# Kernel tuning notes

Hardware: AMD Instinct MI355X
Metric: run time of the kernel (lower is better)

## Reference

```python
import jax, jax.numpy as jnp
import numpy as np

B, C, F, H, W, K = 8, 1, 64, 256, 256, 3
PAD = [(1, 1), (1, 1)]
DN = ('NCHW', 'OIHW', 'NCHW')


def _conv(x, w):
    # Conv2d(1->F, k=3, pad=1, no bias): x [B,1,H,W], w [F,1,3,3] -> [B,F,H,W]
    return jax.lax.conv_general_dilated(x, w, (1, 1), PAD, dimension_numbers=DN)


def _conv_t(u, w):
    # ConvTranspose2d(F->1, k=3, pad=1, stride=1) with shared weight == conv with
    # spatially-flipped kernel, in/out swapped, padding k-1-p = 1.
    wt = jnp.flip(w, axis=(-2, -1)).transpose(1, 0, 2, 3)  # [1,F,3,3]
    return jax.lax.conv_general_dilated(u, wt, (1, 1), PAD, dimension_numbers=DN)


def _op_norm2(w):
    # Power iteration for ||conv_t(conv(.))|| on an image of shape (1,H,W), max 300 iters, tol 1e-4.
    tol = jnp.float32(1e-4)
    x0 = jnp.ones((1, C, H, W), jnp.float32)
    x0 = x0 / jnp.linalg.norm(x0.reshape(-1))

    def cond(s):
        k, x, val, rel = s
        return jnp.logical_and(k < 300, rel >= tol)

    def body(s):
        k, x, val, rel = s
        x2 = _conv_t(_conv(x, w), w)
        v2 = jnp.linalg.norm(x2.reshape(-1))
        r2 = jnp.abs(v2 - val) / val
        return (k + 1, x2 / v2, v2, r2)

    _, _, val, _ = jax.lax.while_loop(
        cond, body, (0, x0, jnp.float32(1.0), jnp.array(jnp.inf, jnp.float32)))
    return jax.lax.stop_gradient(val)  # torch runs this under no_grad


def setup_inputs() -> dict:
    key = jax.random.key(0)
    ks = jax.random.split(key, 6)
    x_in = jax.random.uniform(ks[0], (B, C, H, W), jnp.float32)
    u_in = jax.random.normal(ks[1], (B, F, H, W), jnp.float32)
    bias = jax.random.normal(ks[2], (B, H * W), jnp.float32)
    beta = jnp.ones((1,), jnp.float32)
    lambd = jnp.ones((1,), jnp.float32)
    HtH_diag = jax.random.uniform(ks[3], (H * W,), jnp.float32)
    w = jax.random.normal(ks[4], (F, C, K, K), jnp.float32) * 0.1
    log_sigma = jnp.zeros((1,), jnp.float32)
    return {"x_in": x_in, "u_in": u_in, "bias": bias, "beta": beta,
            "lambd": lambd, "HtH_diag": HtH_diag, "w": w, "log_sigma": log_sigma}


def reference(x_in, u_in, bias, beta, lambd, HtH_diag, w, log_sigma):
    lip2 = _op_norm2(w)
    sigma = jnp.exp(log_sigma) + 0.05                 # [1]
    tau = 0.99 / (beta / 2 + sigma * lip2)            # [1]
    # H_star_H acts on flattened image: diagonal linear operator
    h = (x_in.reshape(x_in.shape[0], -1) * HtH_diag).reshape(x_in.shape)
    Dx = x_in - tau * h - tau * _conv_t(u_in, w) + tau * bias.reshape(x_in.shape)
    output0 = jnp.clip(Dx, 0.0, 1.0)
    Du = 2.0 * sigma * _conv(output0, w) - sigma * _conv(x_in, w) + u_in
    output1 = jnp.clip(Du, -lambd, lambd)
    return (output0, output1)
```

## Files before the change

kernel.cpp:

```cpp
#include <hip/hip_runtime.h>
#include <math.h>

#define IMH 256
#define IMW 256
#define NBT 8
#define NF  64
#define HW  65536

#define TSZ 16
#define MB 10
#define NBATCH 30
#define HALO (2*MB)
#define BROW 68
#define BUFSZ (60*BROW + 8)

#define NG0 8
#define FG0 (NF / NG0)

#define WS_SM   0
#define WS_K5   81
#define WS_ET   106
#define WS_EB   111
#define WS_EL   116
#define WS_ER   121
#define WS_C4   126
#define WS_LIP2 431
#define WS_TAU  432
#define WS_SIGMA 433
#define WS_ST_K    434
#define WS_ST_VAL  435
#define WS_ST_STOP 436

__global__ void setup_kernel(const float* __restrict__ w, float* __restrict__ ws) {
    int t = threadIdx.x;
    __shared__ float smS[81];
    if (t < 81) {
        int a = t / 9, bq = t % 9;
        int dry = a / 3 - 1, drx = a % 3 - 1;
        int dqy = bq / 3 - 1, dqx = bq % 3 - 1;
        int r_idx = (1 - dry) * 3 + (1 - drx);
        int q_idx = (dqy + 1) * 3 + (dqx + 1);
        float s = 0.f;
        for (int f = 0; f < NF; ++f) s += w[f * 9 + r_idx] * w[f * 9 + q_idx];
        smS[t] = s;
        ws[WS_SM + t] = s;
    }
    __syncthreads();
    if (t < 25) {
        int dy = t / 5 - 2, dx = t % 5 - 2;
        float k = 0.f;
        for (int a = 0; a < 9; ++a) {
            int dry = a / 3 - 1, drx = a % 3 - 1;
            for (int bq = 0; bq < 9; ++bq) {
                int dqy = bq / 3 - 1, dqx = bq % 3 - 1;
                if (dry + dqy == dy && drx + dqx == dx) k += smS[a * 9 + bq];
            }
        }
        ws[WS_K5 + t] = k;
    }
    if (t == 0) {
        for (int dd = 0; dd < 5; ++dd) {
            int dx = dd - 2;
            float et = 0.f, eb = 0.f, el = 0.f, er = 0.f;
            for (int dr = -1; dr <= 1; ++dr) {
                int dq = dx - dr;
                if (dq < -1 || dq > 1) continue;
                et += smS[(0 * 3 + dr + 1) * 9 + (2 * 3 + dq + 1)];
                eb += smS[(2 * 3 + dr + 1) * 9 + (0 * 3 + dq + 1)];
                el += smS[((dr + 1) * 3 + 0) * 9 + ((dq + 1) * 3 + 2)];
                er += smS[((dr + 1) * 3 + 2) * 9 + ((dq + 1) * 3 + 0)];
            }
            ws[WS_ET + dd] = et;
            ws[WS_EB + dd] = eb;
            ws[WS_EL + dd] = el;
            ws[WS_ER + dd] = er;
        }
        ws[WS_C4 + 0] = smS[0 * 9 + 8];
        ws[WS_C4 + 1] = smS[2 * 9 + 6];
        ws[WS_C4 + 2] = smS[6 * 9 + 2];
        ws[WS_C4 + 3] = smS[8 * 9 + 0];
        ws[WS_ST_K] = 0.f;
        ws[WS_ST_VAL] = 1.0f;
        ws[WS_ST_STOP] = 0.f;
    }
}

__global__ __launch_bounds__(256) void pi_batch_kernel(
    float* __restrict__ ws, float* __restrict__ gbuf,
    float* __restrict__ part, int batch) {
    __shared__ float bufA[BUFSZ];
    __shared__ float bufB[BUFSZ];
    __shared__ float sred[4];
    const int tid = threadIdx.x;
    const int bid = blockIdx.x;
    const int wid = tid >> 6;
    const int lane = tid & 63;
    const int q = tid & 15;
    const int strip = tid >> 4;
    const int tx = bid & 15;
    const int ty = bid >> 4;
    const float* gin = gbuf + ((batch & 1) ? HW : 0);
    float* gout      = gbuf + ((batch & 1) ? 0 : HW);

    if (batch > 0 && ws[WS_ST_STOP] != 0.f) return;

    if (bid == 0 && batch > 0) {
        float k_it = ws[WS_ST_K];
        float val  = ws[WS_ST_VAL];
        float nprev = 1.0f;
        float newstop = 0.f;
        const float* pb = part + (size_t)((batch - 1) * MB) * 1024;
        for (int s = 0; s < MB; ++s) {
            const float* pp = pb + (size_t)s * 1024;
            float sm = pp[tid] + pp[tid + 256] + pp[tid + 512] + pp[tid + 768];
#pragma unroll
            for (int o = 32; o > 0; o >>= 1) sm += __shfl_down(sm, o, 64);
            if (lane == 0) sred[wid] = sm;
            __syncthreads();
            float tot = sred[0] + sred[1] + sred[2] + sred[3];
            __syncthreads();
            float n = sqrtf(tot);
            float v = n / nprev;
            nprev = n;
            float rel = fabsf(v - val) / val;
            val = v;
            k_it += 1.f;
            if (rel < 1e-4f || k_it >= 300.f) { newstop = 1.f; break; }
        }
        if (tid == 0) {
            ws[WS_ST_K] = k_it;
            ws[WS_ST_VAL] = val;
            ws[WS_ST_STOP] = newstop;
        }
        __syncthreads();
    }

    float k5[25];
#pragma unroll
    for (int i = 0; i < 25; ++i) k5[i] = ws[WS_K5 + i];
    float et[5], eb[5], el[5], er[5], c4[4];
#pragma unroll
    for (int i = 0; i < 5; ++i) {
        et[i] = ws[WS_ET + i]; eb[i] = ws[WS_EB + i];
        el[i] = ws[WS_EL + i]; er[i] = ws[WS_ER + i];
    }
#pragma unroll
    for (int i = 0; i < 4; ++i) c4[i] = ws[WS_C4 + i];

    float inv_n;
    if (batch == 0) {
        inv_n = 1.0f / 256.0f;
    } else {
        const float* pp = part + (size_t)(batch * MB - 1) * 1024;
        float s = pp[tid] + pp[tid + 256] + pp[tid + 512] + pp[tid + 768];
#pragma unroll
        for (int o = 32; o > 0; o >>= 1) s += __shfl_down(s, o, 64);
        if (lane == 0) sred[wid] = s;
        __syncthreads();
        inv_n = 1.0f / sqrtf(sred[0] + sred[1] + sred[2] + sred[3]);
        __syncthreads();
    }

    for (int i = tid; i < BUFSZ; i += 256) {
        float v = 0.f;
        if (i >= 4) {
            int cell = i - 4;
            int r = cell / BROW, c = cell - r * BROW;
            if (r < 60 && c < 64) {
                int gy = ty * 16 - 22 + r;
                int gx = tx * 16 - 24 + c;
                if ((unsigned)gy < IMH && (unsigned)gx < IMW)
                    v = (batch == 0) ? inv_n : gin[gy * IMW + gx] * inv_n;
            }
        }
        bufA[i] = v;
        bufB[i] = 0.f;
    }
    __syncthreads();

    const bool active = (strip < 14);
    const int r0 = 2 + 4 * strip;
    const int gy0 = ty * 16 - 22 + r0;
    const int gx0 = tx * 16 - 24 + 4 * q;
    bool iny[4], bt[4], bb[4];
#pragma unroll
    for (int k = 0; k < 4; ++k) {
        int gy = gy0 + k;
        iny[k] = ((unsigned)gy < IMH);
        bt[k] = (gy == 0);
        bb[k] = (gy == IMH - 1);
    }
    bool inx[4];
#pragma unroll
    for (int i = 0; i < 4; ++i) inx[i] = ((unsigned)(gx0 + i) < IMW);
    const bool bL = (gx0 == 0);
    const bool bR = (gx0 + 3 == IMW - 1);
    const bool central = (q >= 6 && q < 10) && (strip >= 5 && strip < 9);
    const int wrow_lo = 2 + 16 * wid;
    const int wrow_hi = (wrow_lo + 16 < 58) ? wrow_lo + 16 : 58;

    float* cur = bufA;
    float* nxt = bufB;
#pragma unroll 1
    for (int s = 0; s < MB; ++s) {
        float pv = 0.f;
        const int lo = 2 + 2 * (s + 1);
        const int hi = 58 - 2 * (s + 1);
        const bool wave_need = (wrow_lo < hi) && (wrow_hi > lo);
        if (active && wave_need) {
            float win[8][8];
            const int base = 4 + (r0 - 2) * BROW + 4 * q;
#pragma unroll
            for (int m = 0; m < 8; ++m) {
                float4 a = *(const float4*)&cur[base + m * BROW];
                float2 lo2 = *(const float2*)&cur[base + m * BROW - 2];
                float2 hi2 = *(const float2*)&cur[base + m * BROW + 4];
                win[m][0] = lo2.x; win[m][1] = lo2.y;
                win[m][2] = a.x;  win[m][3] = a.y;
                win[m][4] = a.z;  win[m][5] = a.w;
                win[m][6] = hi2.x; win[m][7] = hi2.y;
            }
            float z[4][4];
#pragma unroll
            for (int k = 0; k < 4; ++k) {
#pragma unroll
                for (int i = 0; i < 4; ++i) z[k][i] = 0.f;
#pragma unroll
                for (int j = 0; j < 5; ++j) {
#pragma unroll
                    for (int dx = 0; dx < 5; ++dx) {
                        const float kv = k5[j * 5 + dx];
                        z[k][0] += kv * win[k + j][0 + dx];
                        z[k][1] += kv * win[k + j][1 + dx];
                        z[k][2] += kv * win[k + j][2 + dx];
                        z[k][3] += kv * win[k + j][3 + dx];
                    }
                }
            }
#pragma unroll
            for (int k = 0; k < 4; ++k) {
                if (bt[k]) {
#pragma unroll
                    for (int i = 0; i < 4; ++i) {
                        float c = 0.f;
#pragma unroll
                        for (int d = 0; d < 5; ++d) c += et[d] * win[k + 2][i + d];
                        z[k][i] -= c;
                    }
                }
                if (bb[k]) {
#pragma unroll
                    for (int i = 0; i < 4; ++i) {
                        float c = 0.f;
#pragma unroll
                        for (int d = 0; d < 5; ++d) c += eb[d] * win[k + 2][i + d];
                        z[k][i] -= c;
                    }
                }
            }
            if (bL) {
#pragma unroll
                for (int k = 0; k < 4; ++k) {
                    float c = 0.f;
#pragma unroll
                    for (int j = 0; j < 5; ++j) c += el[j] * win[k + j][2];
                    z[k][0] -= c;
                    if (bt[k]) z[k][0] += c4[0] * win[k + 2][2];
                    if (bb[k]) z[k][0] += c4[2] * win[k + 2][2];
                }
            }
            if (bR) {
#pragma unroll
                for (int k = 0; k < 4; ++k) {
                    float c = 0.f;
#pragma unroll
                    for (int j = 0; j < 5; ++j) c += er[j] * win[k + j][5];
                    z[k][3] -= c;
                    if (bt[k]) z[k][3] += c4[1] * win[k + 2][5];
                    if (bb[k]) z[k][3] += c4[3] * win[k + 2][5];
                }
            }
#pragma unroll
            for (int k = 0; k < 4; ++k) {
                float4 o;
                o.x = (iny[k] && inx[0]) ? z[k][0] : 0.f;
                o.y = (iny[k] && inx[1]) ? z[k][1] : 0.f;
                o.z = (iny[k] && inx[2]) ? z[k][2] : 0.f;
                o.w = (iny[k] && inx[3]) ? z[k][3] : 0.f;
                *(float4*)&nxt[4 + (r0 + k) * BROW + 4 * q] = o;
                if (central)
                    pv += o.x * o.x + o.y * o.y + o.z * o.z + o.w * o.w;
            }
        }
#pragma unroll
        for (int o = 32; o > 0; o >>= 1) pv += __shfl_down(pv, o, 64);
        if (lane == 0)
            part[(size_t)(batch * MB + s) * 1024 + (bid << 2) + wid] = pv;
        __syncthreads();
        float* tmp = cur; cur = nxt; nxt = tmp;
    }

    if (tid < 64) {
        int rr = tid >> 2, cq = tid & 3;
        float4 v = *(const float4*)&cur[4 + (22 + rr) * BROW + 24 + 4 * cq];
        int gy = ty * 16 + rr, gx = tx * 16 + 4 * cq;
        *(float4*)&gout[gy * IMW + gx] = v;
    }
}

__global__ __launch_bounds__(256) void finalize_kernel(
    float* __restrict__ ws, const float* __restrict__ part,
    const float* __restrict__ beta, const float* __restrict__ log_sigma) {
    __shared__ float sr[4];
    const int tid = threadIdx.x;
    const int lane = tid & 63;
    const int wid = tid >> 6;
    float k_it = ws[WS_ST_K];
    float val  = ws[WS_ST_VAL];
    const float stop = ws[WS_ST_STOP];
    if (stop == 0.f) {
        float nprev = 1.0f;
        const float* pb = part + (size_t)((NBATCH - 1) * MB) * 1024;
        for (int s = 0; s < MB; ++s) {
            const float* pp = pb + (size_t)s * 1024;
            float sm = pp[tid] + pp[tid + 256] + pp[tid + 512] + pp[tid + 768];
#pragma unroll
            for (int o = 32; o > 0; o >>= 1) sm += __shfl_down(sm, o, 64);
            if (lane == 0) sr[wid] = sm;
            __syncthreads();
            float tot = sr[0] + sr[1] + sr[2] + sr[3];
            __syncthreads();
            float n = sqrtf(tot);
            float v = n / nprev;
            nprev = n;
            float rel = fabsf(v - val) / val;
            val = v;
            k_it += 1.f;
            if (rel < 1e-4f || k_it >= 300.f) break;
        }
    }
    if (tid == 0) {
        float lip2 = val;
        float sigma = expf(log_sigma[0]) + 0.05f;
        float tau = 0.99f / (beta[0] * 0.5f + sigma * lip2);
        ws[WS_LIP2] = lip2;
        ws[WS_TAU] = tau;
        ws[WS_SIGMA] = sigma;
    }
}

__global__ __launch_bounds__(256) void out0_part_kernel(
    const float* __restrict__ u_in, const float* __restrict__ w,
    float* __restrict__ part0) {
    const int tid = threadIdx.x;
    const int lane = tid & 63;
    const int wid = tid >> 6;
    const int y = blockIdx.x * 4 + wid;
    const int g = blockIdx.y;
    const int b = blockIdx.z;
    const int x0 = lane * 4;
    float4 ct = {0.f, 0.f, 0.f, 0.f};
    const float* ub = u_in + ((size_t)b * NF + g * FG0) * HW;
    const float* wg = w + g * FG0 * 9;
#pragma unroll 4
    for (int f = 0; f < FG0; ++f) {
        const float* uf = ub + (size_t)f * HW;
        const float* wf = wg + f * 9;
#pragma unroll
        for (int dy = -1; dy <= 1; ++dy) {
            int yy = y + dy;
            float4 v = {0.f, 0.f, 0.f, 0.f};
            if ((unsigned)yy < IMH)
                v = *(const float4*)(uf + yy * IMW + x0);
            float m1 = __shfl_up(v.w, 1);
            if (lane == 0) m1 = 0.f;
            float p4 = __shfl_down(v.x, 1);
            if (lane == 63) p4 = 0.f;
            const float w2 = wf[(1 - dy) * 3 + 2];
            const float w1 = wf[(1 - dy) * 3 + 1];
            const float w0 = wf[(1 - dy) * 3 + 0];
            ct.x += w2 * m1  + w1 * v.x + w0 * v.y;
            ct.y += w2 * v.x + w1 * v.y + w0 * v.z;
            ct.z += w2 * v.y + w1 * v.z + w0 * v.w;
            ct.w += w2 * v.z + w1 * v.w + w0 * p4;
        }
    }
    *(float4*)(part0 + ((size_t)(g * NBT + b)) * HW + y * IMW + x0) = ct;
}

__global__ __launch_bounds__(256) void out0_combine_kernel(
    const float* __restrict__ x_in, const float* __restrict__ bias,
    const float* __restrict__ HtH, const float* __restrict__ ws,
    const float* __restrict__ part0, float* __restrict__ out0) {
    const int tid = threadIdx.x;
    const int lane = tid & 63;
    const int wid = tid >> 6;
    const int y = blockIdx.x * 4 + wid;
    const int b = blockIdx.y;
    const int x0 = lane * 4;
    const int p = y * IMW + x0;
    const float tau = ws[WS_TAU];
    float4 ct = {0.f, 0.f, 0.f, 0.f};
#pragma unroll
    for (int g = 0; g < NG0; ++g) {
        const float4 pv = *(const float4*)(part0 + ((size_t)(g * NBT + b)) * HW + p);
        ct.x += pv.x; ct.y += pv.y; ct.z += pv.z; ct.w += pv.w;
    }
    const float4 xi = *(const float4*)(x_in + (size_t)b * HW + p);
    const float4 hh = *(const float4*)(HtH + p);
    const float4 bs = *(const float4*)(bias + (size_t)b * HW + p);
    float4 o;
    o.x = fminf(fmaxf(xi.x - tau * (hh.x * xi.x) - tau * ct.x + tau * bs.x, 0.f), 1.f);
    o.y = fminf(fmaxf(xi.y - tau * (hh.y * xi.y) - tau * ct.y + tau * bs.y, 0.f), 1.f);
    o.z = fminf(fmaxf(xi.z - tau * (hh.z * xi.z) - tau * ct.z + tau * bs.z, 0.f), 1.f);
    o.w = fminf(fmaxf(xi.w - tau * (hh.w * xi.w) - tau * ct.w + tau * bs.w, 0.f), 1.f);
    *(float4*)(out0 + (size_t)b * HW + p) = o;
}

__global__ __launch_bounds__(256) void out1_kernel(
    const float* __restrict__ x_in, const float* __restrict__ u_in,
    const float* __restrict__ lambd, const float* __restrict__ w,
    const float* __restrict__ ws, const float* __restrict__ out0,
    float* __restrict__ out1) {
    const int tid = threadIdx.x;
    const int lane = tid & 63;
    const int wid = tid >> 6;
    const int y = blockIdx.x * 4 + wid;
    const int f = blockIdx.y;
    const int b = blockIdx.z;
    const int x0 = lane * 4;
    const float sigma = ws[WS_SIGMA];
    const float lam = lambd[0];
    const float* wf = w + f * 9;
    float wr[9];
#pragma unroll
    for (int i = 0; i < 9; ++i) wr[i] = wf[i];
    const float* o0 = out0 + (size_t)b * HW;
    const float* xb = x_in + (size_t)b * HW;
    float4 s1 = {0.f, 0.f, 0.f, 0.f};
    float4 s2 = {0.f, 0.f, 0.f, 0.f};
#pragma unroll
    for (int dy = -1; dy <= 1; ++dy) {
        int yy = y + dy;
        float4 a = {0.f, 0.f, 0.f, 0.f};
        float4 c = {0.f, 0.f, 0.f, 0.f};
        if ((unsigned)yy < IMH) {
            a = *(const float4*)(o0 + yy * IMW + x0);
            c = *(const float4*)(xb + yy * IMW + x0);
        }
        float am1 = __shfl_up(a.w, 1);  if (lane == 0) am1 = 0.f;
        float ap4 = __shfl_down(a.x, 1); if (lane == 63) ap4 = 0.f;
        float cm1 = __shfl_up(c.w, 1);  if (lane == 0) cm1 = 0.f;
        float cp4 = __shfl_down(c.x, 1); if (lane == 63) cp4 = 0.f;
        const float w0 = wr[(dy + 1) * 3 + 0];
        const float w1 = wr[(dy + 1) * 3 + 1];
        const float w2 = wr[(dy + 1) * 3 + 2];
        s1.x += w0 * am1 + w1 * a.x + w2 * a.y;
        s1.y += w0 * a.x + w1 * a.y + w2 * a.z;
        s1.z += w0 * a.y + w1 * a.z + w2 * a.w;
        s1.w += w0 * a.z + w1 * a.w + w2 * ap4;
        s2.x += w0 * cm1 + w1 * c.x + w2 * c.y;
        s2.y += w0 * c.x + w1 * c.y + w2 * c.z;
        s2.z += w0 * c.y + w1 * c.z + w2 * c.w;
        s2.w += w0 * c.z + w1 * c.w + w2 * cp4;
    }
    const size_t idx = (size_t)(b * NF + f) * HW + y * IMW + x0;
    const float4 uq = *(const float4*)(u_in + idx);
    float4 o;
    o.x = fminf(fmaxf(2.f * sigma * s1.x - sigma * s2.x + uq.x, -lam), lam);
    o.y = fminf(fmaxf(2.f * sigma * s1.y - sigma * s2.y + uq.y, -lam), lam);
    o.z = fminf(fmaxf(2.f * sigma * s1.z - sigma * s2.z + uq.z, -lam), lam);
    o.w = fminf(fmaxf(2.f * sigma * s1.w - sigma * s2.w + uq.w, -lam), lam);
    *(float4*)(out1 + idx) = o;
}

extern "C" void kernel_launch(void* const* d_in, const int* in_sizes, int n_in,
                              void* d_out, int out_size, void* d_ws, size_t ws_size,
                              hipStream_t stream) {
    const float* x_in = (const float*)d_in[0];
    const float* u_in = (const float*)d_in[1];
    const float* bias = (const float*)d_in[2];
    const float* beta = (const float*)d_in[3];
    const float* lambd = (const float*)d_in[4];
    const float* HtH = (const float*)d_in[5];
    const float* w = (const float*)d_in[6];
    const float* log_sigma = (const float*)d_in[7];
    float* ws = (float*)d_ws;
    float* out0 = (float*)d_out;
    float* out1 = out0 + (size_t)NBT * HW;
    float* gbuf = out1;
    float* part = out1 + 2 * HW;
    float* part0 = part + (size_t)300 * 1024;

    setup_kernel<<<1, 128, 0, stream>>>(w, ws);
    for (int b = 0; b < NBATCH; ++b)
        pi_batch_kernel<<<256, 256, 0, stream>>>(ws, gbuf, part, b);
    finalize_kernel<<<1, 256, 0, stream>>>(ws, part, beta, log_sigma);
    out0_part_kernel<<<dim3(IMH / 4, NG0, NBT), 256, 0, stream>>>(u_in, w, part0);
    out0_combine_kernel<<<dim3(IMH / 4, NBT), 256, 0, stream>>>(x_in, bias, HtH, ws, part0, out0);
    out1_kernel<<<dim3(IMH / 4, NF, NBT), 256, 0, stream>>>(x_in, u_in, lambd, w, ws, out0, out1);
}
```

Baseline: 397.8 us.

## Fold out0 partial conv into power-iteration launches and double PI threads

The separate out0_part_kernel is removed. Its 2048 row-group blocks are now spread across the 30 power-iteration launches as 69 extra blocks each, so that streaming u_in can overlap with the latency-bound stencil iterations. The power-iteration blocks also go from 256 to 512 threads, with each thread computing 2 output rows instead of 4, and the partial-norm layout and reductions widen to match. The risk is that the extra blocks compete with the stencil blocks for CUs and memory bandwidth, and the bigger blocks add reduction and sync overhead.

```diff
diff --git a/kernel.cpp b/kernel.cpp
--- a/kernel.cpp
+++ b/kernel.cpp
@@ -14,8 +14,13 @@
 #define BROW 68
 #define BUFSZ (60*BROW + 8)
 
+#define PIT 512
+#define NPART 2048
+
 #define NG0 8
 #define FG0 (NF / NG0)
+#define OB_TOTAL 2048
+#define OBPB 69
 
 #define WS_SM   0
 #define WS_K5   81
@@ -85,14 +90,58 @@
     }
 }
 
-__global__ __launch_bounds__(256) void pi_batch_kernel(
+__global__ __launch_bounds__(PIT) void pi_batch_kernel(
     float* __restrict__ ws, float* __restrict__ gbuf,
-    float* __restrict__ part, int batch) {
+    float* __restrict__ part, float* __restrict__ part0,
+    const float* __restrict__ u_in, const float* __restrict__ w,
+    int batch) {
     __shared__ float bufA[BUFSZ];
     __shared__ float bufB[BUFSZ];
-    __shared__ float sred[4];
+    __shared__ float sred[8];
     const int tid = threadIdx.x;
     const int bid = blockIdx.x;
+
+    if (bid >= 256) {
+        const int obi = batch * OBPB + (bid - 256);
+        if (obi < OB_TOTAL) {
+            const int yb = obi & 31;
+            const int g = (obi >> 5) & 7;
+            const int b = obi >> 8;
+            const int lane = tid & 63;
+            const int wd = tid >> 6;
+            const int y = yb * 8 + wd;
+            const int x0 = lane * 4;
+            float4 ct = {0.f, 0.f, 0.f, 0.f};
+            const float* ub = u_in + ((size_t)b * NF + g * FG0) * HW;
+            const float* wg = w + g * FG0 * 9;
+#pragma unroll 4
+            for (int f = 0; f < FG0; ++f) {
+                const float* uf = ub + (size_t)f * HW;
+                const float* wf = wg + f * 9;
+#pragma unroll
+                for (int dy = -1; dy <= 1; ++dy) {
+                    int yy = y + dy;
+                    float4 v = {0.f, 0.f, 0.f, 0.f};
+                    if ((unsigned)yy < IMH)
+                        v = *(const float4*)(uf + yy * IMW + x0);
+                    float m1 = __shfl_up(v.w, 1);
+                    if (lane == 0) m1 = 0.f;
+                    float p4 = __shfl_down(v.x, 1);
+                    if (lane == 63) p4 = 0.f;
+                    const float w2 = wf[(1 - dy) * 3 + 2];
+                    const float w1 = wf[(1 - dy) * 3 + 1];
+                    const float w0 = wf[(1 - dy) * 3 + 0];
+                    ct.x += w2 * m1  + w1 * v.x + w0 * v.y;
+                    ct.y += w2 * v.x + w1 * v.y + w0 * v.z;
+                    ct.z += w2 * v.y + w1 * v.z + w0 * v.w;
+                    ct.w += w2 * v.z + w1 * v.w + w0 * p4;
+                }
+            }
+            *(float4*)(part0 + ((size_t)(g * NBT + b)) * HW + y * IMW + x0) = ct;
+        }
+        return;
+    }
+
     const int wid = tid >> 6;
     const int lane = tid & 63;
     const int q = tid & 15;
@@ -109,15 +158,16 @@
         float val  = ws[WS_ST_VAL];
         float nprev = 1.0f;
         float newstop = 0.f;
-        const float* pb = part + (size_t)((batch - 1) * MB) * 1024;
+        const float* pb = part + (size_t)((batch - 1) * MB) * NPART;
         for (int s = 0; s < MB; ++s) {
-            const float* pp = pb + (size_t)s * 1024;
-            float sm = pp[tid] + pp[tid + 256] + pp[tid + 512] + pp[tid + 768];
+            const float* pp = pb + (size_t)s * NPART;
+            float sm = pp[tid] + pp[tid + 512] + pp[tid + 1024] + pp[tid + 1536];
 #pragma unroll
             for (int o = 32; o > 0; o >>= 1) sm += __shfl_down(sm, o, 64);
             if (lane == 0) sred[wid] = sm;
             __syncthreads();
-            float tot = sred[0] + sred[1] + sred[2] + sred[3];
+            float tot = sred[0] + sred[1] + sred[2] + sred[3]
+                      + sred[4] + sred[5] + sred[6] + sred[7];
             __syncthreads();
             float n = sqrtf(tot);
             float v = n / nprev;
@@ -151,17 +201,18 @@
     if (batch == 0) {
         inv_n = 1.0f / 256.0f;
     } else {
-        const float* pp = part + (size_t)(batch * MB - 1) * 1024;
-        float s = pp[tid] + pp[tid + 256] + pp[tid + 512] + pp[tid + 768];
+        const float* pp = part + (size_t)(batch * MB - 1) * NPART;
+        float s = pp[tid] + pp[tid + 512] + pp[tid + 1024] + pp[tid + 1536];
 #pragma unroll
         for (int o = 32; o > 0; o >>= 1) s += __shfl_down(s, o, 64);
         if (lane == 0) sred[wid] = s;
         __syncthreads();
-        inv_n = 1.0f / sqrtf(sred[0] + sred[1] + sred[2] + sred[3]);
+        inv_n = 1.0f / sqrtf(sred[0] + sred[1] + sred[2] + sred[3]
+                           + sred[4] + sred[5] + sred[6] + sred[7]);
         __syncthreads();
     }
 
-    for (int i = tid; i < BUFSZ; i += 256) {
+    for (int i = tid; i < BUFSZ; i += PIT) {
         float v = 0.f;
         if (i >= 4) {
             int cell = i - 4;
@@ -178,13 +229,13 @@
     }
     __syncthreads();
 
-    const bool active = (strip < 14);
-    const int r0 = 2 + 4 * strip;
+    const bool active = (strip < 28);
+    const int r0 = 2 + 2 * strip;
     const int gy0 = ty * 16 - 22 + r0;
     const int gx0 = tx * 16 - 24 + 4 * q;
-    bool iny[4], bt[4], bb[4];
-#pragma unroll
-    for (int k = 0; k < 4; ++k) {
+    bool iny[2], bt[2], bb[2];
+#pragma unroll
+    for (int k = 0; k < 2; ++k) {
         int gy = gy0 + k;
         iny[k] = ((unsigned)gy < IMH);
         bt[k] = (gy == 0);
@@ -195,9 +246,9 @@
     for (int i = 0; i < 4; ++i) inx[i] = ((unsigned)(gx0 + i) < IMW);
     const bool bL = (gx0 == 0);
     const bool bR = (gx0 + 3 == IMW - 1);
-    const bool central = (q >= 6 && q < 10) && (strip >= 5 && strip < 9);
-    const int wrow_lo = 2 + 16 * wid;
-    const int wrow_hi = (wrow_lo + 16 < 58) ? wrow_lo + 16 : 58;
+    const bool central = (q >= 6 && q < 10) && (strip >= 10 && strip < 18);
+    const int wrow_lo = 2 + 8 * wid;
+    const int wrow_hi = (wrow_lo + 8 < 58) ? wrow_lo + 8 : 58;
 
     float* cur = bufA;
     float* nxt = bufB;
@@ -208,10 +259,10 @@
         const int hi = 58 - 2 * (s + 1);
         const bool wave_need = (wrow_lo < hi) && (wrow_hi > lo);
         if (active && wave_need) {
-            float win[8][8];
+            float win[6][8];
             const int base = 4 + (r0 - 2) * BROW + 4 * q;
 #pragma unroll
-            for (int m = 0; m < 8; ++m) {
+            for (int m = 0; m < 6; ++m) {
                 float4 a = *(const float4*)&cur[base + m * BROW];
                 float2 lo2 = *(const float2*)&cur[base + m * BROW - 2];
                 float2 hi2 = *(const float2*)&cur[base + m * BROW + 4];
@@ -220,9 +271,9 @@
                 win[m][4] = a.z;  win[m][5] = a.w;
                 win[m][6] = hi2.x; win[m][7] = hi2.y;
             }
-            float z[4][4];
-#pragma unroll
-            for (int k = 0; k < 4; ++k) {
+            float z[2][4];
+#pragma unroll
+            for (int k = 0; k < 2; ++k) {
 #pragma unroll
                 for (int i = 0; i < 4; ++i) z[k][i] = 0.f;
 #pragma unroll
@@ -238,7 +289,7 @@
                 }
             }
 #pragma unroll
-            for (int k = 0; k < 4; ++k) {
+            for (int k = 0; k < 2; ++k) {
                 if (bt[k]) {
 #pragma unroll
                     for (int i = 0; i < 4; ++i) {
@@ -260,7 +311,7 @@
             }
             if (bL) {
 #pragma unroll
-                for (int k = 0; k < 4; ++k) {
+                for (int k = 0; k < 2; ++k) {
                     float c = 0.f;
 #pragma unroll
                     for (int j = 0; j < 5; ++j) c += el[j] * win[k + j][2];
@@ -271,7 +322,7 @@
             }
             if (bR) {
 #pragma unroll
-                for (int k = 0; k < 4; ++k) {
+                for (int k = 0; k < 2; ++k) {
                     float c = 0.f;
 #pragma unroll
                     for (int j = 0; j < 5; ++j) c += er[j] * win[k + j][5];
@@ -281,7 +332,7 @@
                 }
             }
 #pragma unroll
-            for (int k = 0; k < 4; ++k) {
+            for (int k = 0; k < 2; ++k) {
                 float4 o;
                 o.x = (iny[k] && inx[0]) ? z[k][0] : 0.f;
                 o.y = (iny[k] && inx[1]) ? z[k][1] : 0.f;
@@ -295,7 +346,7 @@
 #pragma unroll
         for (int o = 32; o > 0; o >>= 1) pv += __shfl_down(pv, o, 64);
         if (lane == 0)
-            part[(size_t)(batch * MB + s) * 1024 + (bid << 2) + wid] = pv;
+            part[(size_t)(batch * MB + s) * NPART + (bid << 3) + wid] = pv;
         __syncthreads();
         float* tmp = cur; cur = nxt; nxt = tmp;
     }
@@ -320,10 +371,12 @@
     const float stop = ws[WS_ST_STOP];
     if (stop == 0.f) {
         float nprev = 1.0f;
-        const float* pb = part + (size_t)((NBATCH - 1) * MB) * 1024;
+        const float* pb = part + (size_t)((NBATCH - 1) * MB) * NPART;
         for (int s = 0; s < MB; ++s) {
-            const float* pp = pb + (size_t)s * 1024;
-            float sm = pp[tid] + pp[tid + 256] + pp[tid + 512] + pp[tid + 768];
+            const float* pp = pb + (size_t)s * NPART;
+            float sm = 0.f;
+#pragma unroll
+            for (int j = 0; j < 8; ++j) sm += pp[tid + 256 * j];
 #pragma unroll
             for (int o = 32; o > 0; o >>= 1) sm += __shfl_down(sm, o, 64);
             if (lane == 0) sr[wid] = sm;
@@ -347,45 +400,6 @@
         ws[WS_TAU] = tau;
         ws[WS_SIGMA] = sigma;
     }
-}
-
-__global__ __launch_bounds__(256) void out0_part_kernel(
-    const float* __restrict__ u_in, const float* __restrict__ w,
-    float* __restrict__ part0) {
-    const int tid = threadIdx.x;
-    const int lane = tid & 63;
-    const int wid = tid >> 6;
-    const int y = blockIdx.x * 4 + wid;
-    const int g = blockIdx.y;
-    const int b = blockIdx.z;
-    const int x0 = lane * 4;
-    float4 ct = {0.f, 0.f, 0.f, 0.f};
-    const float* ub = u_in + ((size_t)b * NF + g * FG0) * HW;
-    const float* wg = w + g * FG0 * 9;
-#pragma unroll 4
-    for (int f = 0; f < FG0; ++f) {
-        const float* uf = ub + (size_t)f * HW;
-        const float* wf = wg + f * 9;
-#pragma unroll
-        for (int dy = -1; dy <= 1; ++dy) {
-            int yy = y + dy;
-            float4 v = {0.f, 0.f, 0.f, 0.f};
-            if ((unsigned)yy < IMH)
-                v = *(const float4*)(uf + yy * IMW + x0);
-            float m1 = __shfl_up(v.w, 1);
-            if (lane == 0) m1 = 0.f;
-            float p4 = __shfl_down(v.x, 1);
-            if (lane == 63) p4 = 0.f;
-            const float w2 = wf[(1 - dy) * 3 + 2];
-            const float w1 = wf[(1 - dy) * 3 + 1];
-            const float w0 = wf[(1 - dy) * 3 + 0];
-            ct.x += w2 * m1  + w1 * v.x + w0 * v.y;
-            ct.y += w2 * v.x + w1 * v.y + w0 * v.z;
-            ct.z += w2 * v.y + w1 * v.z + w0 * v.w;
-            ct.w += w2 * v.z + w1 * v.w + w0 * p4;
-        }
-    }
-    *(float4*)(part0 + ((size_t)(g * NBT + b)) * HW + y * IMW + x0) = ct;
 }
 
 __global__ __launch_bounds__(256) void out0_combine_kernel(
@@ -490,13 +504,12 @@
     float* out1 = out0 + (size_t)NBT * HW;
     float* gbuf = out1;
     float* part = out1 + 2 * HW;
-    float* part0 = part + (size_t)300 * 1024;
+    float* part0 = part + (size_t)300 * NPART;
 
     setup_kernel<<<1, 128, 0, stream>>>(w, ws);
     for (int b = 0; b < NBATCH; ++b)
-        pi_batch_kernel<<<256, 256, 0, stream>>>(ws, gbuf, part, b);
+        pi_batch_kernel<<<256 + OBPB, PIT, 0, stream>>>(ws, gbuf, part, part0, u_in, w, b);
     finalize_kernel<<<1, 256, 0, stream>>>(ws, part, beta, log_sigma);
-    out0_part_kernel<<<dim3(IMH / 4, NG0, NBT), 256, 0, stream>>>(u_in, w, part0);
     out0_combine_kernel<<<dim3(IMH / 4, NBT), 256, 0, stream>>>(x_in, bias, HtH, ws, part0, out0);
     out1_kernel<<<dim3(IMH / 4, NF, NBT), 256, 0, stream>>>(x_in, u_in, lambd, w, ws, out0, out1);
 }
```

Result: slower. 668.8 us (+68.1%).
